# Kernel optimization log

Measured on AMD Instinct MI355X. Metric: run time of the kernel, lower is better.

The kernel has to match this reference:

```python
import jax, jax.numpy as jnp
import numpy as np

H = 16  # nhead


def setup_inputs() -> dict:
    key = jax.random.key(0)
    ks = jax.random.split(key, 10)
    B, N, D = 2, 2048, 1024
    n_ctx = 1024
    P = 256
    s = lambda fan: 1.0 / np.sqrt(fan)
    return {
        "x": jax.random.normal(ks[0], (B, N, D), jnp.float32),
        "n_ctx": n_ctx,
        "ctx_ppr": jax.random.uniform(ks[1], (n_ctx,), jnp.float32),
        "ctx_delta": jax.random.normal(ks[2], (n_ctx, P), jnp.float32),
        "ctx_trust": jax.random.normal(ks[3], (n_ctx,), jnp.float32),
        "W_in": jax.random.normal(ks[4], (3 * D, D), jnp.float32) * s(D),
        "b_in": jnp.zeros((3 * D,), jnp.float32),
        "W_out": jax.random.normal(ks[5], (D, D), jnp.float32) * s(D),
        "b_out": jnp.zeros((D,), jnp.float32),
        "log_ppr_alpha": jnp.full((1,), 0.1, jnp.float32),
        "trust_scale": jnp.full((1,), 0.1, jnp.float32),
        "Wd1": jax.random.normal(ks[6], (D // 2, P), jnp.float32) * s(P),
        "bd1": jnp.zeros((D // 2,), jnp.float32),
        "Wd2": jax.random.normal(ks[7], (1, D // 2), jnp.float32) * 0.01,
        "bd2": jnp.zeros((1,), jnp.float32),
    }


def reference(x, n_ctx, ctx_ppr, ctx_delta, ctx_trust, W_in, b_in, W_out, b_out,
              log_ppr_alpha, trust_scale, Wd1, bd1, Wd2, bd2):
    B, N, D = x.shape
    d = D // H
    scale = d ** -0.5

    qkv = x @ W_in.T + b_in                       # [B,N,3D]
    q, k, v = jnp.split(qkv, 3, axis=-1)
    to_heads = lambda t: t.reshape(B, N, H, d).transpose(0, 2, 1, 3)  # [B,H,N,d]
    q, k, v = to_heads(q), to_heads(k), to_heads(v)

    # sigmoid value gate on context keys
    gate = jax.nn.sigmoid(trust_scale * ctx_trust)           # [n_ctx]
    gate_full = jnp.concatenate([gate, jnp.ones(N - n_ctx, x.dtype)])
    v = v * gate_full[None, None, :, None]

    logits = jnp.einsum('bhqd,bhkd->bhqk', q, k) * scale     # [B,H,N,N]

    # additive per-key bias: alpha*log(ppr) + delta MLP
    ppr_bias = log_ppr_alpha * jnp.log(jnp.clip(ctx_ppr, 1e-8))
    h = jax.nn.gelu(ctx_delta @ Wd1.T + bd1, approximate=False)
    delta_bias = (h @ Wd2.T + bd2)[:, 0]                     # [n_ctx]
    col_bias = jnp.concatenate([ppr_bias + delta_bias, jnp.zeros(N - n_ctx, x.dtype)])
    logits = logits + col_bias[None, None, None, :]

    weights = jax.nn.softmax(logits, axis=-1)
    out = jnp.einsum('bhqk,bhkd->bhqd', weights, v)
    out = out.transpose(0, 2, 1, 3).reshape(B, N, D)
    return out @ W_out.T + b_out
```

## Files before the change

kernel.cpp:

```cpp
#include <hip/hip_runtime.h>
#include <hip/hip_bf16.h>
#include <hip/hip_fp16.h>
#include <math.h>


#define NTOK 2048
#define DMODEL 1024
#define NHEAD 16
#define DHEAD 64
#define NCTX 1024
#define BTOT 4096

typedef __attribute__((ext_vector_type(8))) short    s8v;
typedef __attribute__((ext_vector_type(8))) _Float16 h8v;
typedef __attribute__((ext_vector_type(4))) float    f4v;
typedef __attribute__((ext_vector_type(4))) ushort   us4;
typedef __attribute__((ext_vector_type(8))) ushort   us8;

__device__ __forceinline__ ushort f2bf(float x) {
    unsigned b = __float_as_uint(x);
    return (ushort)((b + 0x7FFFu + ((b >> 16) & 1u)) >> 16);
}
__device__ __forceinline__ float bf2f(ushort u) {
    return __uint_as_float(((unsigned)u) << 16);
}
__device__ __forceinline__ ushort f2h(float x) {
    return __half_as_ushort(__float2half_rn(x));
}

#define GLDS16(gsrc, ldst) __builtin_amdgcn_global_load_lds(                              \
    (__attribute__((address_space(1))) unsigned int*)(gsrc),                              \
    (__attribute__((address_space(3))) unsigned int*)(ldst), 16, 0, 0)

__global__ __launch_bounds__(256)
void bias_kernel(const float* __restrict__ ctx_ppr, const float* __restrict__ ctx_delta,
                 const float* __restrict__ ctx_trust,
                 const float* __restrict__ alpha, const float* __restrict__ tscale,
                 const float* __restrict__ Wd1, const float* __restrict__ bd1,
                 const float* __restrict__ Wd2, const float* __restrict__ bd2,
                 float* __restrict__ gate_full, float* __restrict__ col_bias)
{
    const int i = blockIdx.x;
    const int t = threadIdx.x;
    if (i >= NCTX) {
        if (t == 0) { gate_full[i] = 1.0f; col_bias[i] = 0.0f; }
        return;
    }
    __shared__ float drow[256];
    __shared__ float red[256];
    drow[t] = ctx_delta[i * 256 + t];
    __syncthreads();

    float partial = 0.0f;
    #pragma unroll
    for (int jj = 0; jj < 2; jj++) {
        const int j = t + jj * 256;
        float s = bd1[j];
        const float4* wrow = (const float4*)&Wd1[j * 256];
        const float4* dr   = (const float4*)drow;
        #pragma unroll 8
        for (int p = 0; p < 64; p++) {
            float4 w = wrow[p], dd = dr[p];
            s += w.x * dd.x + w.y * dd.y + w.z * dd.z + w.w * dd.w;
        }
        float g = 0.5f * s * (1.0f + erff(s * 0.70710678118654752f));
        partial += g * Wd2[j];
    }
    red[t] = partial;
    __syncthreads();
    for (int off = 128; off > 0; off >>= 1) {
        if (t < off) red[t] += red[t + off];
        __syncthreads();
    }
    if (t == 0) {
        float ppr = fmaxf(ctx_ppr[i], 1e-8f);
        col_bias[i]  = alpha[0] * logf(ppr) + (red[0] + bd2[0]);
        gate_full[i] = 1.0f / (1.0f + __expf(-(tscale[0] * ctx_trust[i])));
    }
}

__global__ __launch_bounds__(256)
void cvt_split(const float* __restrict__ in, ushort* __restrict__ hi,
               ushort* __restrict__ lo, int n4)
{
    for (int i = blockIdx.x * 256 + threadIdx.x; i < n4; i += gridDim.x * 256) {
        float4 v = ((const float4*)in)[i];
        us4 h, l; ushort hb;
        hb = f2bf(v.x); h[0] = hb; l[0] = f2bf(v.x - bf2f(hb));
        hb = f2bf(v.y); h[1] = hb; l[1] = f2bf(v.y - bf2f(hb));
        hb = f2bf(v.z); h[2] = hb; l[2] = f2bf(v.z - bf2f(hb));
        hb = f2bf(v.w); h[3] = hb; l[3] = f2bf(v.w - bf2f(hb));
        ((us4*)hi)[i] = h; ((us4*)lo)[i] = l;
    }
}

__global__ __launch_bounds__(256)
void cvt_f16(const float* __restrict__ in, ushort* __restrict__ out16, int n4)
{
    for (int i = blockIdx.x * 256 + threadIdx.x; i < n4; i += gridDim.x * 256) {
        float4 v = ((const float4*)in)[i];
        us4 h;
        h[0] = f2h(v.x); h[1] = f2h(v.y); h[2] = f2h(v.z); h[3] = f2h(v.w);
        ((us4*)out16)[i] = h;
    }
}

__global__ __launch_bounds__(256, 3)
void gemm_f16(const ushort* __restrict__ Af, const ushort* __restrict__ Bf,
              const float* __restrict__ bias,
              ushort* __restrict__ qf, ushort* __restrict__ kf,
              ushort* __restrict__ vtf,
              const float* __restrict__ gate_full, int M, int N, int K)
{
    __shared__ ushort AS[4096], BS[4096];

    const int t = threadIdx.x, lane = t & 63, wid = t >> 6;
    const int l15 = lane & 15, l4 = lane >> 4;
    const int wr = wid >> 1, wc = wid & 1;

    const int nwg = gridDim.x * gridDim.y;
    const int lin = blockIdx.y * gridDim.x + blockIdx.x;
    const int w   = (lin & 7) * (nwg >> 3) + (lin >> 3);
    const int bx  = w % gridDim.x, by = w / gridDim.x;
    const int m0 = by * 128, n0 = bx * 128;

    f4v acc[4][4];
    #pragma unroll
    for (int mi = 0; mi < 4; mi++)
        #pragma unroll
        for (int nj = 0; nj < 4; nj++)
            #pragma unroll
            for (int r = 0; r < 4; r++) acc[mi][nj][r] = 0.0f;

    const int srow_l = lane >> 2;
    const int schunk = (lane & 3) ^ ((lane >> 2) & 3) ^ ((lane >> 4) & 3);
    const int rch = l4 ^ (l15 & 3) ^ ((l15 >> 2) & 3);

    const ushort* sp = (wid < 2) ? Af : Bf;
    ushort* dp = (wid < 2) ? AS : BS;
    const int wofs = (wid & 1) * 64;
    const int base0 = (wid < 2) ? m0 : n0;

    for (int k0 = 0; k0 < K; k0 += 32) {
        __syncthreads();
        #pragma unroll
        for (int i = 0; i < 4; i++) {
            const int row = wofs + i * 16 + srow_l;
            GLDS16(sp + (size_t)(base0 + row) * K + k0 + schunk * 8,
                   dp + ((wid & 1) * 4 + i) * 512);
        }
        __syncthreads();

        h8v af[4], bf[4];
        #pragma unroll
        for (int mi = 0; mi < 4; mi++) {
            const int row = wr * 64 + mi * 16 + l15;
            af[mi] = *(const h8v*)&AS[row * 32 + rch * 8];
        }
        #pragma unroll
        for (int nj = 0; nj < 4; nj++) {
            const int row = wc * 64 + nj * 16 + l15;
            bf[nj] = *(const h8v*)&BS[row * 32 + rch * 8];
        }
        #pragma unroll
        for (int mi = 0; mi < 4; mi++)
            #pragma unroll
            for (int nj = 0; nj < 4; nj++)
                acc[mi][nj] = __builtin_amdgcn_mfma_f32_16x16x32_f16(af[mi], bf[nj], acc[mi][nj], 0, 0, 0);
    }

    const int sec = n0 >> 10;
    #pragma unroll
    for (int mi = 0; mi < 4; mi++) {
        const int mbase = m0 + wr * 64 + mi * 16 + l4 * 4;
        const int bb = mbase >> 11, tok0 = mbase & 2047;
        #pragma unroll
        for (int nj = 0; nj < 4; nj++) {
            const int n = n0 + wc * 64 + nj * 16 + l15;
            const float bn = bias[n];
            const int rem = n & 1023, h = rem >> 6, jd = rem & 63;
            if (sec == 2) {
                us4 hv;
                #pragma unroll
                for (int r = 0; r < 4; r++)
                    hv[r] = f2h((acc[mi][nj][r] + bn) * gate_full[tok0 + r]);
                const size_t vb = ((size_t)((bb << 4) + h) * 64 + jd) * NTOK + tok0;
                *(us4*)&vtf[vb] = hv;
            } else {
                ushort* dst = sec ? kf : qf;
                #pragma unroll
                for (int r = 0; r < 4; r++) {
                    const size_t idx = ((size_t)((bb << 4) + h) * NTOK + (tok0 + r)) * 64 + jd;
                    dst[idx] = f2h(acc[mi][nj][r] + bn);
                }
            }
        }
    }
}

template<int MT, int EPI>
__global__ __launch_bounds__(256)
void gemm_mfma(const ushort* __restrict__ Ah, const ushort* __restrict__ Al,
               const ushort* __restrict__ Bh, const ushort* __restrict__ Bl,
               const float* __restrict__ bias, float* __restrict__ C,
               const float* __restrict__ gate_full, int M, int N, int K)
{
    constexpr int BM = MT * 32;
    __shared__ ushort AhS[BM * 32], AlS[BM * 32], BhS[4096], BlS[4096];

    const int t = threadIdx.x, lane = t & 63, wid = t >> 6;
    const int l15 = lane & 15, l4 = lane >> 4;
    const int wr = wid >> 1, wc = wid & 1;

    const int nwg = gridDim.x * gridDim.y;
    const int lin = blockIdx.y * gridDim.x + blockIdx.x;
    const int w   = (lin & 7) * (nwg >> 3) + (lin >> 3);
    const int bx  = w % gridDim.x, by = w / gridDim.x;
    const int m0 = by * BM, n0 = bx * 128;

    f4v acc[MT][4];
    #pragma unroll
    for (int mi = 0; mi < MT; mi++)
        #pragma unroll
        for (int nj = 0; nj < 4; nj++)
            #pragma unroll
            for (int r = 0; r < 4; r++) acc[mi][nj][r] = 0.0f;

    const int srow_l = lane >> 2;
    const int schunk = (lane & 3) ^ ((lane >> 2) & 3) ^ ((lane >> 4) & 3);
    const int rch = l4 ^ (l15 & 3) ^ ((l15 >> 2) & 3);

    const ushort* sA = (wid == 0) ? Ah : Al;
    const ushort* sB = (wid == 2) ? Bh : Bl;
    ushort* dA = (wid == 0) ? AhS : AlS;
    ushort* dB = (wid == 2) ? BhS : BlS;

    for (int k0 = 0; k0 < K; k0 += 32) {
        __syncthreads();
        if (wid < 2) {
            #pragma unroll
            for (int i = 0; i < BM / 16; i++) {
                const int row = i * 16 + srow_l;
                GLDS16(sA + (size_t)(m0 + row) * K + k0 + schunk * 8, dA + i * 512);
            }
        } else {
            #pragma unroll
            for (int i = 0; i < 8; i++) {
                const int row = i * 16 + srow_l;
                GLDS16(sB + (size_t)(n0 + row) * K + k0 + schunk * 8, dB + i * 512);
            }
        }
        __syncthreads();

        s8v afh[MT], afl[MT], bfh[4], bfl[4];
        #pragma unroll
        for (int mi = 0; mi < MT; mi++) {
            const int row = wr * (MT * 16) + mi * 16 + l15;
            afh[mi] = *(const s8v*)&AhS[row * 32 + rch * 8];
            afl[mi] = *(const s8v*)&AlS[row * 32 + rch * 8];
        }
        #pragma unroll
        for (int nj = 0; nj < 4; nj++) {
            const int row = wc * 64 + nj * 16 + l15;
            bfh[nj] = *(const s8v*)&BhS[row * 32 + rch * 8];
            bfl[nj] = *(const s8v*)&BlS[row * 32 + rch * 8];
        }
        #pragma unroll
        for (int mi = 0; mi < MT; mi++)
            #pragma unroll
            for (int nj = 0; nj < 4; nj++) {
                acc[mi][nj] = __builtin_amdgcn_mfma_f32_16x16x32_bf16(afh[mi], bfh[nj], acc[mi][nj], 0, 0, 0);
                acc[mi][nj] = __builtin_amdgcn_mfma_f32_16x16x32_bf16(afh[mi], bfl[nj], acc[mi][nj], 0, 0, 0);
                acc[mi][nj] = __builtin_amdgcn_mfma_f32_16x16x32_bf16(afl[mi], bfh[nj], acc[mi][nj], 0, 0, 0);
            }
    }

    #pragma unroll
    for (int mi = 0; mi < MT; mi++) {
        #pragma unroll
        for (int nj = 0; nj < 4; nj++) {
            const int n = n0 + wc * 64 + nj * 16 + l15;
            const float bn = bias[n];
            #pragma unroll
            for (int r = 0; r < 4; r++) {
                const int m = m0 + wr * (MT * 16) + mi * 16 + l4 * 4 + r;
                C[(size_t)m * N + n] = acc[mi][nj][r] + bn;
            }
        }
    }
}

__global__ __launch_bounds__(256, 4)
void attn_f16(const ushort* __restrict__ qfp, const ushort* __restrict__ kfp,
              const ushort* __restrict__ vtf, const float* __restrict__ col_bias,
              ushort* __restrict__ atth, ushort* __restrict__ attl)
{
    __shared__ ushort KS[2][4096];
    __shared__ ushort VS[2][4096];
    __shared__ float  CBS[2][64];

    const int t = threadIdx.x, lane = t & 63, wid = t >> 6;
    const int lin = blockIdx.y * gridDim.x + blockIdx.x;
    const int w   = (lin & 7) * 128 + (lin >> 3);
    const int bh  = w >> 5, qt = w & 31;

    const size_t qkbase = (size_t)bh * (NTOK * DHEAD);
    const size_t vtbase = (size_t)bh * (DHEAD * NTOK);
    const int l15 = lane & 15, l4 = lane >> 4;
    const int q0 = qt * 64 + wid * 16;

    h8v qf[2];
    #pragma unroll
    for (int s = 0; s < 2; s++)
        qf[s] = *(const h8v*)&qfp[qkbase + (size_t)(q0 + l15) * 64 + 32 * s + 8 * l4];

    f4v oacc[4];
    #pragma unroll
    for (int f = 0; f < 4; f++)
        #pragma unroll
        for (int r = 0; r < 4; r++) oacc[f][r] = 0.0f;
    float mreg = -INFINITY;
    float sreg = 0.0f;

    us8 vreg[4];
    const int vj = lane & 7, vdh0 = lane >> 3;
    const int k0c  = 4 * (vj >> 2) + 2 * (vj & 1);
    const int off0 = ((vj >> 1) & 1) * 8;

    #define STAGE_K(nb, kt) do {                                                          \
        _Pragma("unroll")                                                                 \
        for (int i_ = 0; i_ < 4; i_++) {                                                  \
            const int row_ = wid * 32 + i_ * 8 + (lane >> 3);                             \
            const int sc_  = ((lane & 7) ^ (row_ & 7)) * 8;                               \
            GLDS16(kfp + qkbase + (size_t)((kt) + row_) * 64 + sc_,                       \
                   &KS[nb][0] + (wid * 4 + i_) * 512);                                    \
        }                                                                                 \
        if (wid == 0 && lane < 16) GLDS16(col_bias + (kt) + lane * 4, &CBS[nb][0]);       \
    } while (0)

    #define LOAD_V(kt) do {                                                               \
        _Pragma("unroll")                                                                 \
        for (int i_ = 0; i_ < 4; i_++) {                                                  \
            const int dh_ = (wid - 2) * 32 + 8 * i_ + vdh0;                               \
            vreg[i_] = *(const us8*)&vtf[vtbase + (size_t)dh_ * NTOK + (kt) + 8 * vj];    \
        }                                                                                 \
    } while (0)

    #define STORE_V(nb) do {                                                              \
        char* dp_ = (char*)&VS[nb][0];                                                    \
        _Pragma("unroll")                                                                 \
        for (int i_ = 0; i_ < 4; i_++) {                                                  \
            const int dh_ = (wid - 2) * 32 + 8 * i_ + vdh0;                               \
            const int b0_ = dh_ * 128 + ((k0c ^ (dh_ & 7)) * 16) + off0;                  \
            const int b1_ = dh_ * 128 + (((k0c + 1) ^ (dh_ & 7)) * 16) + off0;            \
            us4 lo4_, hi4_;                                                               \
            lo4_[0] = vreg[i_][0]; lo4_[1] = vreg[i_][1];                                 \
            lo4_[2] = vreg[i_][2]; lo4_[3] = vreg[i_][3];                                 \
            hi4_[0] = vreg[i_][4]; hi4_[1] = vreg[i_][5];                                 \
            hi4_[2] = vreg[i_][6]; hi4_[3] = vreg[i_][7];                                 \
            *(us4*)(dp_ + b0_) = lo4_;                                                    \
            *(us4*)(dp_ + b1_) = hi4_;                                                    \
        }                                                                                 \
    } while (0)

    if (wid < 2) STAGE_K(0, 0); else { LOAD_V(0); STORE_V(0); }
    __syncthreads();

    int cur = 0;
    for (int kt = 0; kt < 32; kt++) {
        const int nxt = cur ^ 1;
        if (kt < 31) { if (wid < 2) STAGE_K(nxt, (kt + 1) * 64); else LOAD_V((kt + 1) * 64); }

        f4v sa[4];
        #pragma unroll
        for (int g = 0; g < 4; g++)
            #pragma unroll
            for (int r = 0; r < 4; r++) sa[g][r] = 0.0f;
        __builtin_amdgcn_s_setprio(1);
        #pragma unroll
        for (int s = 0; s < 2; s++) {
            #pragma unroll
            for (int g = 0; g < 4; g++) {
                const int row = 16 * g + l15;
                const int idx = row * 64 + (((4 * s + l4) ^ (l15 & 7))) * 8;
                h8v kfr = *(const h8v*)&KS[cur][idx];
                sa[g] = __builtin_amdgcn_mfma_f32_16x16x32_f16(kfr, qf[s], sa[g], 0, 0, 0);
            }
        }
        __builtin_amdgcn_s_setprio(0);

        float sv[4][4], smax = -INFINITY;
        #pragma unroll
        for (int g = 0; g < 4; g++)
            #pragma unroll
            for (int r = 0; r < 4; r++) {
                const float x = sa[g][r] * 0.125f + CBS[cur][16 * g + 4 * l4 + r];
                sv[g][r] = x;
                smax = fmaxf(smax, x);
            }
        if (__any(smax > mreg + 8.0f)) {
            float mx = smax;
            mx = fmaxf(mx, __shfl_xor(mx, 16));
            mx = fmaxf(mx, __shfl_xor(mx, 32));
            const float mnew = fmaxf(mreg, mx);
            const float fs = __expf(mreg - mnew);
            mreg = mnew;
            sreg *= fs;
            float fq[4];
            #pragma unroll
            for (int r = 0; r < 4; r++) fq[r] = __shfl(fs, 4 * l4 + r);
            #pragma unroll
            for (int f = 0; f < 4; f++)
                #pragma unroll
                for (int r = 0; r < 4; r++) oacc[f][r] *= fq[r];
        }

        union H8 { h8v v; __half2 h2[4]; };
        H8 pa[2];
        {
            float pv[4][4];
            float acc_s = 0.0f;
            #pragma unroll
            for (int g = 0; g < 4; g++)
                #pragma unroll
                for (int r = 0; r < 4; r++) {
                    const float p = __expf(sv[g][r] - mreg);
                    pv[g][r] = p;
                    acc_s += p;
                }
            sreg += acc_s;
            #pragma unroll
            for (int s = 0; s < 2; s++)
                #pragma unroll
                for (int a = 0; a < 2; a++) {
                    const int g = 2 * s + a;
                    pa[s].h2[2 * a]     = __float22half2_rn(make_float2(pv[g][0], pv[g][1]));
                    pa[s].h2[2 * a + 1] = __float22half2_rn(make_float2(pv[g][2], pv[g][3]));
                }
        }

        __builtin_amdgcn_s_setprio(1);
        #pragma unroll
        for (int s = 0; s < 2; s++) {
            #pragma unroll
            for (int f = 0; f < 4; f++) {
                const int row = 16 * f + l15;
                const int idx = row * 64 + (((4 * s + l4) ^ (l15 & 7))) * 8;
                h8v vfr = *(const h8v*)&VS[cur][idx];
                oacc[f] = __builtin_amdgcn_mfma_f32_16x16x32_f16(pa[s].v, vfr, oacc[f], 0, 0, 0);
            }
        }
        __builtin_amdgcn_s_setprio(0);

        if (kt < 31 && wid >= 2) STORE_V(nxt);
        __syncthreads();
        cur = nxt;
    }

    const int b = bh >> 4, h = bh & 15;
    {
        float ts = sreg;
        ts += __shfl_xor(ts, 16);
        ts += __shfl_xor(ts, 32);
        const float inv = 1.0f / ts;
        float invq[4];
        #pragma unroll
        for (int r = 0; r < 4; r++) invq[r] = __shfl(inv, 4 * l4 + r);
        #pragma unroll
        for (int r = 0; r < 4; r++) {
            const int q = q0 + 4 * l4 + r;
            const size_t o = ((size_t)(b * NTOK + q)) * DMODEL + h * DHEAD + l15;
            #pragma unroll
            for (int f = 0; f < 4; f++) {
                const float v = oacc[f][r] * invq[r];
                const ushort hb = f2bf(v);
                atth[o + 16 * f] = hb;
                attl[o + 16 * f] = f2bf(v - bf2f(hb));
            }
        }
    }
    #undef STAGE_K
    #undef LOAD_V
    #undef STORE_V
}

extern "C" void kernel_launch(void* const* d_in, const int* in_sizes, int n_in,
                              void* d_out, int out_size, void* d_ws, size_t ws_size,
                              hipStream_t stream)
{
    const float* x         = (const float*)d_in[0];
    const float* ctx_ppr   = (const float*)d_in[2];
    const float* ctx_delta = (const float*)d_in[3];
    const float* ctx_trust = (const float*)d_in[4];
    const float* W_in      = (const float*)d_in[5];
    const float* b_in      = (const float*)d_in[6];
    const float* W_out     = (const float*)d_in[7];
    const float* b_out     = (const float*)d_in[8];
    const float* alpha     = (const float*)d_in[9];
    const float* tscale    = (const float*)d_in[10];
    const float* Wd1       = (const float*)d_in[11];
    const float* bd1       = (const float*)d_in[12];
    const float* Wd2       = (const float*)d_in[13];
    const float* bd2       = (const float*)d_in[14];
    float* out = (float*)d_out;

    float* ws = (float*)d_ws;
    float* gate_full = ws;
    float* col_bias  = ws + 2048;
    ushort* u = (ushort*)(ws + 4096);
    ushort* xf   = u;  u += 4194304;
    ushort* wif  = u;  u += 3145728;
    ushort* woh  = u;  u += 1048576;
    ushort* wol  = u;  u += 1048576;
    ushort* qf   = u;  u += 4194304;
    ushort* kf   = u;  u += 4194304;
    ushort* vtf  = u;  u += 4194304;
    ushort* atth = u;  u += 4194304;
    ushort* attl = u;  u += 4194304;

    bias_kernel<<<NTOK, 256, 0, stream>>>(ctx_ppr, ctx_delta, ctx_trust, alpha, tscale,
                                          Wd1, bd1, Wd2, bd2, gate_full, col_bias);
    cvt_f16<<<1024, 256, 0, stream>>>(x,    xf,  1048576);
    cvt_f16<<<768,  256, 0, stream>>>(W_in, wif, 786432);
    cvt_split<<<256, 256, 0, stream>>>(W_out, woh, wol, 262144);

    gemm_f16<<<dim3(24, 32), 256, 0, stream>>>(xf, wif, b_in, qf, kf, vtf, gate_full,
                                               BTOT, 3 * DMODEL, DMODEL);
    attn_f16<<<dim3(32, 32), 256, 0, stream>>>(qf, kf, vtf, col_bias, atth, attl);
    gemm_mfma<2, 0><<<dim3(8, 64), 256, 0, stream>>>(atth, attl, woh, wol, b_out, out,
                                                     nullptr, BTOT, DMODEL, DMODEL);
}
```

Measured before the change: 296.7 us.

## Use single fp16 for output projection and merge conversion kernels

The output projection previously ran three bf16 MFMAs per tile on hi/lo split operands, with the attention kernel writing split bf16 outputs. It now runs a single fp16 MFMA path: attention writes one fp16 buffer, W_out is converted to fp16, and both GEMMs share one templated kernel. The three conversion launches are merged into one. This cuts output-GEMM MFMA work roughly threefold and halves attention-output traffic, at the cost of lower precision in the final projection.

```diff
diff --git a/kernel.cpp b/kernel.cpp
--- a/kernel.cpp
+++ b/kernel.cpp
@@ -11,19 +11,11 @@
 #define NCTX 1024
 #define BTOT 4096
 
-typedef __attribute__((ext_vector_type(8))) short    s8v;
 typedef __attribute__((ext_vector_type(8))) _Float16 h8v;
 typedef __attribute__((ext_vector_type(4))) float    f4v;
 typedef __attribute__((ext_vector_type(4))) ushort   us4;
 typedef __attribute__((ext_vector_type(8))) ushort   us8;
 
-__device__ __forceinline__ ushort f2bf(float x) {
-    unsigned b = __float_as_uint(x);
-    return (ushort)((b + 0x7FFFu + ((b >> 16) & 1u)) >> 16);
-}
-__device__ __forceinline__ float bf2f(ushort u) {
-    return __uint_as_float(((unsigned)u) << 16);
-}
 __device__ __forceinline__ ushort f2h(float x) {
     return __half_as_ushort(__float2half_rn(x));
 }
@@ -80,133 +72,32 @@
 }
 
 __global__ __launch_bounds__(256)
-void cvt_split(const float* __restrict__ in, ushort* __restrict__ hi,
-               ushort* __restrict__ lo, int n4)
+void cvt_all(const float* __restrict__ x, const float* __restrict__ wi,
+             const float* __restrict__ wo,
+             ushort* __restrict__ xf, ushort* __restrict__ wif, ushort* __restrict__ wof)
 {
-    for (int i = blockIdx.x * 256 + threadIdx.x; i < n4; i += gridDim.x * 256) {
-        float4 v = ((const float4*)in)[i];
-        us4 h, l; ushort hb;
-        hb = f2bf(v.x); h[0] = hb; l[0] = f2bf(v.x - bf2f(hb));
-        hb = f2bf(v.y); h[1] = hb; l[1] = f2bf(v.y - bf2f(hb));
-        hb = f2bf(v.z); h[2] = hb; l[2] = f2bf(v.z - bf2f(hb));
-        hb = f2bf(v.w); h[3] = hb; l[3] = f2bf(v.w - bf2f(hb));
-        ((us4*)hi)[i] = h; ((us4*)lo)[i] = l;
-    }
-}
-
-__global__ __launch_bounds__(256)
-void cvt_f16(const float* __restrict__ in, ushort* __restrict__ out16, int n4)
-{
-    for (int i = blockIdx.x * 256 + threadIdx.x; i < n4; i += gridDim.x * 256) {
-        float4 v = ((const float4*)in)[i];
+    for (int i = blockIdx.x * 256 + threadIdx.x; i < 2097152; i += gridDim.x * 256) {
+        const float* src; ushort* dst; int j;
+        if (i < 1048576)      { src = x;  dst = xf;  j = i; }
+        else if (i < 1835008) { src = wi; dst = wif; j = i - 1048576; }
+        else                  { src = wo; dst = wof; j = i - 1835008; }
+        float4 v = ((const float4*)src)[j];
         us4 h;
         h[0] = f2h(v.x); h[1] = f2h(v.y); h[2] = f2h(v.z); h[3] = f2h(v.w);
-        ((us4*)out16)[i] = h;
-    }
-}
-
+        ((us4*)dst)[j] = h;
+    }
+}
+
+template<int MT, int EPI>
 __global__ __launch_bounds__(256, 3)
 void gemm_f16(const ushort* __restrict__ Af, const ushort* __restrict__ Bf,
-              const float* __restrict__ bias,
+              const float* __restrict__ bias, float* __restrict__ C,
               ushort* __restrict__ qf, ushort* __restrict__ kf,
               ushort* __restrict__ vtf,
               const float* __restrict__ gate_full, int M, int N, int K)
 {
-    __shared__ ushort AS[4096], BS[4096];
-
-    const int t = threadIdx.x, lane = t & 63, wid = t >> 6;
-    const int l15 = lane & 15, l4 = lane >> 4;
-    const int wr = wid >> 1, wc = wid & 1;
-
-    const int nwg = gridDim.x * gridDim.y;
-    const int lin = blockIdx.y * gridDim.x + blockIdx.x;
-    const int w   = (lin & 7) * (nwg >> 3) + (lin >> 3);
-    const int bx  = w % gridDim.x, by = w / gridDim.x;
-    const int m0 = by * 128, n0 = bx * 128;
-
-    f4v acc[4][4];
-    #pragma unroll
-    for (int mi = 0; mi < 4; mi++)
-        #pragma unroll
-        for (int nj = 0; nj < 4; nj++)
-            #pragma unroll
-            for (int r = 0; r < 4; r++) acc[mi][nj][r] = 0.0f;
-
-    const int srow_l = lane >> 2;
-    const int schunk = (lane & 3) ^ ((lane >> 2) & 3) ^ ((lane >> 4) & 3);
-    const int rch = l4 ^ (l15 & 3) ^ ((l15 >> 2) & 3);
-
-    const ushort* sp = (wid < 2) ? Af : Bf;
-    ushort* dp = (wid < 2) ? AS : BS;
-    const int wofs = (wid & 1) * 64;
-    const int base0 = (wid < 2) ? m0 : n0;
-
-    for (int k0 = 0; k0 < K; k0 += 32) {
-        __syncthreads();
-        #pragma unroll
-        for (int i = 0; i < 4; i++) {
-            const int row = wofs + i * 16 + srow_l;
-            GLDS16(sp + (size_t)(base0 + row) * K + k0 + schunk * 8,
-                   dp + ((wid & 1) * 4 + i) * 512);
-        }
-        __syncthreads();
-
-        h8v af[4], bf[4];
-        #pragma unroll
-        for (int mi = 0; mi < 4; mi++) {
-            const int row = wr * 64 + mi * 16 + l15;
-            af[mi] = *(const h8v*)&AS[row * 32 + rch * 8];
-        }
-        #pragma unroll
-        for (int nj = 0; nj < 4; nj++) {
-            const int row = wc * 64 + nj * 16 + l15;
-            bf[nj] = *(const h8v*)&BS[row * 32 + rch * 8];
-        }
-        #pragma unroll
-        for (int mi = 0; mi < 4; mi++)
-            #pragma unroll
-            for (int nj = 0; nj < 4; nj++)
-                acc[mi][nj] = __builtin_amdgcn_mfma_f32_16x16x32_f16(af[mi], bf[nj], acc[mi][nj], 0, 0, 0);
-    }
-
-    const int sec = n0 >> 10;
-    #pragma unroll
-    for (int mi = 0; mi < 4; mi++) {
-        const int mbase = m0 + wr * 64 + mi * 16 + l4 * 4;
-        const int bb = mbase >> 11, tok0 = mbase & 2047;
-        #pragma unroll
-        for (int nj = 0; nj < 4; nj++) {
-            const int n = n0 + wc * 64 + nj * 16 + l15;
-            const float bn = bias[n];
-            const int rem = n & 1023, h = rem >> 6, jd = rem & 63;
-            if (sec == 2) {
-                us4 hv;
-                #pragma unroll
-                for (int r = 0; r < 4; r++)
-                    hv[r] = f2h((acc[mi][nj][r] + bn) * gate_full[tok0 + r]);
-                const size_t vb = ((size_t)((bb << 4) + h) * 64 + jd) * NTOK + tok0;
-                *(us4*)&vtf[vb] = hv;
-            } else {
-                ushort* dst = sec ? kf : qf;
-                #pragma unroll
-                for (int r = 0; r < 4; r++) {
-                    const size_t idx = ((size_t)((bb << 4) + h) * NTOK + (tok0 + r)) * 64 + jd;
-                    dst[idx] = f2h(acc[mi][nj][r] + bn);
-                }
-            }
-        }
-    }
-}
-
-template<int MT, int EPI>
-__global__ __launch_bounds__(256)
-void gemm_mfma(const ushort* __restrict__ Ah, const ushort* __restrict__ Al,
-               const ushort* __restrict__ Bh, const ushort* __restrict__ Bl,
-               const float* __restrict__ bias, float* __restrict__ C,
-               const float* __restrict__ gate_full, int M, int N, int K)
-{
     constexpr int BM = MT * 32;
-    __shared__ ushort AhS[BM * 32], AlS[BM * 32], BhS[4096], BlS[4096];
+    __shared__ ushort AS[BM * 32], BS[4096];
 
     const int t = threadIdx.x, lane = t & 63, wid = t >> 6;
     const int l15 = lane & 15, l4 = lane >> 4;
@@ -230,61 +121,83 @@
     const int schunk = (lane & 3) ^ ((lane >> 2) & 3) ^ ((lane >> 4) & 3);
     const int rch = l4 ^ (l15 & 3) ^ ((l15 >> 2) & 3);
 
-    const ushort* sA = (wid == 0) ? Ah : Al;
-    const ushort* sB = (wid == 2) ? Bh : Bl;
-    ushort* dA = (wid == 0) ? AhS : AlS;
-    ushort* dB = (wid == 2) ? BhS : BlS;
-
     for (int k0 = 0; k0 < K; k0 += 32) {
         __syncthreads();
         if (wid < 2) {
             #pragma unroll
-            for (int i = 0; i < BM / 16; i++) {
-                const int row = i * 16 + srow_l;
-                GLDS16(sA + (size_t)(m0 + row) * K + k0 + schunk * 8, dA + i * 512);
+            for (int i = 0; i < MT; i++) {
+                const int row = (wid & 1) * (MT * 16) + i * 16 + srow_l;
+                GLDS16(Af + (size_t)(m0 + row) * K + k0 + schunk * 8,
+                       AS + ((wid & 1) * MT + i) * 512);
             }
         } else {
             #pragma unroll
-            for (int i = 0; i < 8; i++) {
-                const int row = i * 16 + srow_l;
-                GLDS16(sB + (size_t)(n0 + row) * K + k0 + schunk * 8, dB + i * 512);
+            for (int i = 0; i < 4; i++) {
+                const int row = (wid & 1) * 64 + i * 16 + srow_l;
+                GLDS16(Bf + (size_t)(n0 + row) * K + k0 + schunk * 8,
+                       BS + ((wid & 1) * 4 + i) * 512);
             }
         }
         __syncthreads();
 
-        s8v afh[MT], afl[MT], bfh[4], bfl[4];
+        h8v af[MT], bf[4];
         #pragma unroll
         for (int mi = 0; mi < MT; mi++) {
             const int row = wr * (MT * 16) + mi * 16 + l15;
-            afh[mi] = *(const s8v*)&AhS[row * 32 + rch * 8];
-            afl[mi] = *(const s8v*)&AlS[row * 32 + rch * 8];
+            af[mi] = *(const h8v*)&AS[row * 32 + rch * 8];
         }
         #pragma unroll
         for (int nj = 0; nj < 4; nj++) {
             const int row = wc * 64 + nj * 16 + l15;
-            bfh[nj] = *(const s8v*)&BhS[row * 32 + rch * 8];
-            bfl[nj] = *(const s8v*)&BlS[row * 32 + rch * 8];
+            bf[nj] = *(const h8v*)&BS[row * 32 + rch * 8];
         }
         #pragma unroll
         for (int mi = 0; mi < MT; mi++)
             #pragma unroll
+            for (int nj = 0; nj < 4; nj++)
+                acc[mi][nj] = __builtin_amdgcn_mfma_f32_16x16x32_f16(af[mi], bf[nj], acc[mi][nj], 0, 0, 0);
+    }
+
+    if (EPI == 0) {
+        #pragma unroll
+        for (int mi = 0; mi < MT; mi++) {
+            #pragma unroll
             for (int nj = 0; nj < 4; nj++) {
-                acc[mi][nj] = __builtin_amdgcn_mfma_f32_16x16x32_bf16(afh[mi], bfh[nj], acc[mi][nj], 0, 0, 0);
-                acc[mi][nj] = __builtin_amdgcn_mfma_f32_16x16x32_bf16(afh[mi], bfl[nj], acc[mi][nj], 0, 0, 0);
-                acc[mi][nj] = __builtin_amdgcn_mfma_f32_16x16x32_bf16(afl[mi], bfh[nj], acc[mi][nj], 0, 0, 0);
-            }
-    }
-
-    #pragma unroll
-    for (int mi = 0; mi < MT; mi++) {
-        #pragma unroll
-        for (int nj = 0; nj < 4; nj++) {
-            const int n = n0 + wc * 64 + nj * 16 + l15;
-            const float bn = bias[n];
-            #pragma unroll
-            for (int r = 0; r < 4; r++) {
-                const int m = m0 + wr * (MT * 16) + mi * 16 + l4 * 4 + r;
-                C[(size_t)m * N + n] = acc[mi][nj][r] + bn;
+                const int n = n0 + wc * 64 + nj * 16 + l15;
+                const float bn = bias[n];
+                #pragma unroll
+                for (int r = 0; r < 4; r++) {
+                    const int m = m0 + wr * (MT * 16) + mi * 16 + l4 * 4 + r;
+                    C[(size_t)m * N + n] = acc[mi][nj][r] + bn;
+                }
+            }
+        }
+    } else {
+        const int sec = n0 >> 10;
+        #pragma unroll
+        for (int mi = 0; mi < MT; mi++) {
+            const int mbase = m0 + wr * (MT * 16) + mi * 16 + l4 * 4;
+            const int bb = mbase >> 11, tok0 = mbase & 2047;
+            #pragma unroll
+            for (int nj = 0; nj < 4; nj++) {
+                const int n = n0 + wc * 64 + nj * 16 + l15;
+                const float bn = bias[n];
+                const int rem = n & 1023, h = rem >> 6, jd = rem & 63;
+                if (sec == 2) {
+                    us4 hv;
+                    #pragma unroll
+                    for (int r = 0; r < 4; r++)
+                        hv[r] = f2h((acc[mi][nj][r] + bn) * gate_full[tok0 + r]);
+                    const size_t vb = ((size_t)((bb << 4) + h) * 64 + jd) * NTOK + tok0;
+                    *(us4*)&vtf[vb] = hv;
+                } else {
+                    ushort* dst = sec ? kf : qf;
+                    #pragma unroll
+                    for (int r = 0; r < 4; r++) {
+                        const size_t idx = ((size_t)((bb << 4) + h) * NTOK + (tok0 + r)) * 64 + jd;
+                        dst[idx] = f2h(acc[mi][nj][r] + bn);
+                    }
+                }
             }
         }
     }
@@ -293,7 +206,7 @@
 __global__ __launch_bounds__(256, 4)
 void attn_f16(const ushort* __restrict__ qfp, const ushort* __restrict__ kfp,
               const ushort* __restrict__ vtf, const float* __restrict__ col_bias,
-              ushort* __restrict__ atth, ushort* __restrict__ attl)
+              ushort* __restrict__ attf)
 {
     __shared__ ushort KS[2][4096];
     __shared__ ushort VS[2][4096];
@@ -471,12 +384,8 @@
             const int q = q0 + 4 * l4 + r;
             const size_t o = ((size_t)(b * NTOK + q)) * DMODEL + h * DHEAD + l15;
             #pragma unroll
-            for (int f = 0; f < 4; f++) {
-                const float v = oacc[f][r] * invq[r];
-                const ushort hb = f2bf(v);
-                atth[o + 16 * f] = hb;
-                attl[o + 16 * f] = f2bf(v - bf2f(hb));
-            }
+            for (int f = 0; f < 4; f++)
+                attf[o + 16 * f] = f2h(oacc[f][r] * invq[r]);
         }
     }
     #undef STAGE_K
@@ -510,23 +419,21 @@
     ushort* u = (ushort*)(ws + 4096);
     ushort* xf   = u;  u += 4194304;
     ushort* wif  = u;  u += 3145728;
-    ushort* woh  = u;  u += 1048576;
-    ushort* wol  = u;  u += 1048576;
+    ushort* wof  = u;  u += 1048576;
     ushort* qf   = u;  u += 4194304;
     ushort* kf   = u;  u += 4194304;
     ushort* vtf  = u;  u += 4194304;
-    ushort* atth = u;  u += 4194304;
-    ushort* attl = u;  u += 4194304;
+    ushort* attf = u;  u += 4194304;
 
     bias_kernel<<<NTOK, 256, 0, stream>>>(ctx_ppr, ctx_delta, ctx_trust, alpha, tscale,
                                           Wd1, bd1, Wd2, bd2, gate_full, col_bias);
-    cvt_f16<<<1024, 256, 0, stream>>>(x,    xf,  1048576);
-    cvt_f16<<<768,  256, 0, stream>>>(W_in, wif, 786432);
-    cvt_split<<<256, 256, 0, stream>>>(W_out, woh, wol, 262144);
-
-    gemm_f16<<<dim3(24, 32), 256, 0, stream>>>(xf, wif, b_in, qf, kf, vtf, gate_full,
-                                               BTOT, 3 * DMODEL, DMODEL);
-    attn_f16<<<dim3(32, 32), 256, 0, stream>>>(qf, kf, vtf, col_bias, atth, attl);
-    gemm_mfma<2, 0><<<dim3(8, 64), 256, 0, stream>>>(atth, attl, woh, wol, b_out, out,
-                                                     nullptr, BTOT, DMODEL, DMODEL);
-}
+    cvt_all<<<2048, 256, 0, stream>>>(x, W_in, W_out, xf, wif, wof);
+
+    gemm_f16<4, 1><<<dim3(24, 32), 256, 0, stream>>>(xf, wif, b_in, nullptr,
+                                                     qf, kf, vtf, gate_full,
+                                                     BTOT, 3 * DMODEL, DMODEL);
+    attn_f16<<<dim3(32, 32), 256, 0, stream>>>(qf, kf, vtf, col_bias, attf);
+    gemm_f16<2, 0><<<dim3(8, 64), 256, 0, stream>>>(attf, wof, b_out, out,
+                                                    nullptr, nullptr, nullptr, nullptr,
+                                                    BTOT, DMODEL, DMODEL);
+}
```

Measured after the change: 275.2 us. 7.2% less time.
